# Optimization experiments

Measured on AMD Instinct MI355X. Metric: run time of the kernel, lower is better.

The kernel has to match this reference:

```python
import jax, jax.numpy as jnp
import numpy as np

N, E = 50000, 400000
F_IN, F_E = 128, 32
H, C = 4, 64          # heads, out_channels per head (concat=False -> head mean)
NUM_CLASSES = 16
BN_EPS = 1e-5


def setup_inputs() -> dict:
    key = jax.random.key(0)
    ks = jax.random.split(key, 16)
    s = 0.05
    return {
        "x": jax.random.normal(ks[0], (N, F_IN), jnp.float32),
        "edge_index": jax.random.randint(ks[1], (2, E), 0, N, jnp.int64),
        "edge_attr": jax.random.normal(ks[2], (E, F_E), jnp.float32),
        # TransformerConv params
        "Wq": jax.random.normal(ks[3], (F_IN, H * C), jnp.float32) * s,
        "bq": jnp.zeros((H * C,), jnp.float32),
        "Wk": jax.random.normal(ks[4], (F_IN, H * C), jnp.float32) * s,
        "bk": jnp.zeros((H * C,), jnp.float32),
        "Wv": jax.random.normal(ks[5], (F_IN, H * C), jnp.float32) * s,
        "bv": jnp.zeros((H * C,), jnp.float32),
        "We": jax.random.normal(ks[6], (F_E, H * C), jnp.float32) * s,  # lin_edge, no bias
        "Wskip": jax.random.normal(ks[7], (F_IN, C), jnp.float32) * s,   # root weight (concat=False -> C)
        "bskip": jnp.zeros((C,), jnp.float32),
        # BatchNorm1d (eval mode: running stats)
        "gamma": jnp.ones((C,), jnp.float32),
        "beta": jnp.zeros((C,), jnp.float32),
        "run_mean": jnp.zeros((C,), jnp.float32),
        "run_var": jnp.ones((C,), jnp.float32),
        # classifier
        "Wc": jax.random.normal(ks[8], (C, NUM_CLASSES), jnp.float32) * s,
        "bc": jnp.zeros((NUM_CLASSES,), jnp.float32),
    }


def reference(x, edge_index, edge_attr, Wq, bq, Wk, bk, Wv, bv, We,
              Wskip, bskip, gamma, beta, run_mean, run_var, Wc, bc):
    src = edge_index[0]  # j (message source)
    dst = edge_index[1]  # i (message target / softmax segment)

    q = (x @ Wq + bq).reshape(N, H, C)
    k = (x @ Wk + bk).reshape(N, H, C)
    v = (x @ Wv + bv).reshape(N, H, C)
    e = (edge_attr @ We).reshape(E, H, C)

    k_j = k[src] + e                                   # [E,H,C]
    score = jnp.sum(q[dst] * k_j, axis=-1) / jnp.sqrt(jnp.float32(C))  # [E,H]

    # segment softmax over incoming edges of each destination node
    m = jax.ops.segment_max(score, dst, num_segments=N)      # [N,H]
    ex = jnp.exp(score - m[dst])                             # [E,H]
    denom = jax.ops.segment_sum(ex, dst, num_segments=N)[dst]
    alpha = ex / denom                                       # [E,H]

    msg = (v[src] + e) * alpha[..., None]                    # [E,H,C]
    out = jax.ops.segment_sum(msg, dst, num_segments=N)      # [N,H,C]
    out = out.mean(axis=1)                                   # concat=False -> head mean [N,C]
    out = out + x @ Wskip + bskip                            # root/skip connection

    out = jax.nn.relu(out)
    # dropout: eval mode -> identity
    out = (out - run_mean) / jnp.sqrt(run_var + BN_EPS) * gamma + beta
    return out @ Wc + bc
```

## Files before the change

### kernel.cpp

```cpp
#include <hip/hip_runtime.h>
#include <hip/hip_bf16.h>

#define H 4
#define C 64
#define HC 256
#define FIN 128
#define FE 32
#define NCLS 16
#define BN_EPS 1e-5f
#define WCOLS 960

typedef __hip_bfloat16 bf16;
typedef __attribute__((ext_vector_type(8))) short short8v;
typedef __attribute__((ext_vector_type(4))) short short4v;
typedef __attribute__((ext_vector_type(2))) short short2v;
typedef __attribute__((ext_vector_type(4))) float floatx4;

__device__ __forceinline__ float b2f(bf16 v) { return __bfloat162float(v); }
__device__ __forceinline__ float bs2f(short s) {
    unsigned u = ((unsigned)(unsigned short)s) << 16;
    return __uint_as_float(u);
}
__device__ __forceinline__ short f2bs(float f) {
    bf16 h = __float2bfloat16(f);
    return *reinterpret_cast<short*>(&h);
}

__global__ __launch_bounds__(128) void pack_w_kernel(
    const float* __restrict__ Wq, const float* __restrict__ Wk, const float* __restrict__ Wv,
    const float* __restrict__ We, const float* __restrict__ Wskip,
    const float* __restrict__ bq, const float* __restrict__ bk, const float* __restrict__ bv,
    const float* __restrict__ bskip,
    const float* __restrict__ gamma, const float* __restrict__ beta,
    const float* __restrict__ rmean, const float* __restrict__ rvar,
    const float* __restrict__ Wc,
    short* __restrict__ Wt, float* __restrict__ bias,
    short* __restrict__ Wet, short* __restrict__ Wct,
    float* __restrict__ scalev, float* __restrict__ shiftv)
{
    const int bid = blockIdx.x;
    const int t = threadIdx.x;
    if (bid < WCOLS) {
        const int col = bid;
        float val, b = 0.f;
        if (col < 256)      { val = Wq[t * HC + col]; b = bq[col]; }
        else if (col < 512) { val = Wk[t * HC + col - 256]; b = bk[col - 256]; }
        else if (col < 768) { val = Wv[t * HC + col - 512]; b = bv[col - 512]; }
        else if (col < 896) {
            int j = col - 768, h = j >> 5, f = j & 31;
            float acc = 0.f;
#pragma unroll 8
            for (int c = 0; c < C; ++c) acc += Wq[t * HC + h * C + c] * We[f * HC + h * C + c];
            val = acc;
            acc = 0.f;
            for (int c = 0; c < C; ++c) acc += bq[h * C + c] * We[f * HC + h * C + c];
            b = acc;
        }
        else { int c2 = col - 896; val = Wskip[t * C + c2]; b = bskip[c2]; }
        Wt[(size_t)col * FIN + t] = f2bs(val);
        if (t == 0) bias[col] = b;
    } else if (bid < WCOLS + 64) {
        const int c2 = bid - WCOLS;
        const int f = t & 31, h = t >> 5;
        Wet[(size_t)c2 * FIN + t] = f2bs(We[f * HC + h * C + c2]);
    } else if (bid < WCOLS + 64 + NCLS) {
        const int cls = bid - WCOLS - 64;
        if (t < C) Wct[(size_t)cls * C + t] = f2bs(Wc[t * NCLS + cls]);
    } else {
        if (t < C) {
            float inv = rsqrtf(rvar[t] + BN_EPS);
            float sc = gamma[t] * inv;
            scalev[t] = sc;
            shiftv[t] = beta[t] - rmean[t] * sc;
        }
    }
}

__global__ __launch_bounds__(256) void qkv_mfma_kernel(
    const float* __restrict__ x, const short* __restrict__ Wt,
    const float* __restrict__ bias,
    bf16* __restrict__ q, unsigned char* __restrict__ kv,
    bf16* __restrict__ qWe, bf16* __restrict__ skip, int N)
{
    const int wid = threadIdx.x >> 6;
    const int lane = threadIdx.x & 63;
    const int n0 = blockIdx.x * 32;
    const int arow = lane & 15, agrp = lane >> 4;
    __shared__ __align__(16) unsigned char kvs[32][512];

    short8v afrag[2][4];
#pragma unroll
    for (int rt = 0; rt < 2; ++rt) {
        int nA = n0 + rt * 16 + arow; if (nA >= N) nA = N - 1;
        const float* xrow = x + (size_t)nA * FIN + agrp * 8;
#pragma unroll
        for (int ks = 0; ks < 4; ++ks) {
            floatx4 x0 = *(const floatx4*)(xrow + ks * 32);
            floatx4 x1 = *(const floatx4*)(xrow + ks * 32 + 4);
            short8v a;
            a[0] = f2bs(x0[0]); a[1] = f2bs(x0[1]); a[2] = f2bs(x0[2]); a[3] = f2bs(x0[3]);
            a[4] = f2bs(x1[0]); a[5] = f2bs(x1[1]); a[6] = f2bs(x1[2]); a[7] = f2bs(x1[3]);
            afrag[rt][ks] = a;
        }
    }

    for (int ct = wid; ct < WCOLS / 16; ct += 4) {
        const int col0 = ct * 16;
        const int col = col0 + arow;
        const short* wp = Wt + (size_t)col * FIN + agrp * 8;
        short8v bfr[4];
#pragma unroll
        for (int ks = 0; ks < 4; ++ks) bfr[ks] = *(const short8v*)(wp + ks * 32);
        floatx4 acc0 = {0.f, 0.f, 0.f, 0.f};
        floatx4 acc1 = {0.f, 0.f, 0.f, 0.f};
#pragma unroll
        for (int ks = 0; ks < 4; ++ks) {
            acc0 = __builtin_amdgcn_mfma_f32_16x16x32_bf16(afrag[0][ks], bfr[ks], acc0, 0, 0, 0);
            acc1 = __builtin_amdgcn_mfma_f32_16x16x32_bf16(afrag[1][ks], bfr[ks], acc1, 0, 0, 0);
        }
        const float bb = bias[col];
#pragma unroll
        for (int rt = 0; rt < 2; ++rt) {
            const floatx4 acc = rt ? acc1 : acc0;
#pragma unroll
            for (int r = 0; r < 4; ++r) {
                const int row = rt * 16 + agrp * 4 + r;
                const int n = n0 + row;
                const float val = acc[r] + bb;
                if (col0 >= 256 && col0 < 768) {
                    int c = col - 256;
                    const int isv = (c >= 256) ? 4 : 0;
                    c &= 255;
                    const int pos = ((c >> 6) * 16 + ((c & 63) >> 2)) * 8 + (c & 3) + isv;
                    const int p8 = __builtin_amdgcn_cvt_pk_fp8_f32(val, val, 0, false);
                    kvs[row][pos] = (unsigned char)(p8 & 0xff);
                } else if (n < N) {
                    if (col0 < 256)      q[(size_t)n * HC + col]          = __float2bfloat16(val);
                    else if (col0 < 896) qWe[(size_t)n * 128 + col - 768] = __float2bfloat16(val);
                    else                 skip[(size_t)n * C + col - 896]  = __float2bfloat16(val);
                }
            }
        }
    }
    __syncthreads();
    const int t = threadIdx.x;
#pragma unroll
    for (int it = 0; it < 4; ++it) {
        const int lin = it * 256 + t;
        const int row = lin >> 5;
        const int ch  = lin & 31;
        const int n = n0 + row;
        if (n < N)
            *(uint4*)(kv + (size_t)n * 512 + ch * 16) = *(const uint4*)(&kvs[row][ch * 16]);
    }
}

__global__ __launch_bounds__(256) void hist_kernel(
    const int* __restrict__ dst, int* __restrict__ deg, int E)
{
    const int i = blockIdx.x * 256 + threadIdx.x;
    if (i < E) atomicAdd(&deg[dst[i]], 1);
}

__global__ __launch_bounds__(256) void partial_kernel(
    const int* __restrict__ deg, int* __restrict__ partials, int N)
{
    const int t = threadIdx.x;
    const int base = blockIdx.x * 1024 + t * 4;
    int s = 0;
#pragma unroll
    for (int i = 0; i < 4; ++i) {
        int idx = base + i;
        if (idx < N) s += deg[idx];
    }
#pragma unroll
    for (int off = 1; off < 64; off <<= 1) s += __shfl_xor(s, off, 64);
    __shared__ int ws[4];
    if ((t & 63) == 0) ws[t >> 6] = s;
    __syncthreads();
    if (t == 0) partials[blockIdx.x] = ws[0] + ws[1] + ws[2] + ws[3];
}

__global__ __launch_bounds__(256) void scan_partials_kernel(
    int* __restrict__ partials, int* __restrict__ rowptr, int nb, int N)
{
    const int t = threadIdx.x;
    __shared__ int sm[256];
    int v = (t < nb) ? partials[t] : 0;
    sm[t] = v;
    __syncthreads();
    for (int off = 1; off < 256; off <<= 1) {
        int vv = (t >= off) ? sm[t - off] : 0;
        __syncthreads();
        sm[t] += vv;
        __syncthreads();
    }
    if (t < nb) partials[t] = sm[t] - v;
    if (t == 255) rowptr[N] = sm[255];
}

__global__ __launch_bounds__(256) void write_rowptr_kernel(
    const int* __restrict__ deg, const int* __restrict__ partials,
    int* __restrict__ rowptr, int N)
{
    const int t = threadIdx.x;
    const int base = blockIdx.x * 1024 + t * 4;
    int d[4];
    int s = 0;
#pragma unroll
    for (int i = 0; i < 4; ++i) {
        int idx = base + i;
        d[i] = (idx < N) ? deg[idx] : 0;
        s += d[i];
    }
    __shared__ int sm[256];
    sm[t] = s;
    __syncthreads();
    for (int off = 1; off < 256; off <<= 1) {
        int vv = (t >= off) ? sm[t - off] : 0;
        __syncthreads();
        sm[t] += vv;
        __syncthreads();
    }
    int run = partials[blockIdx.x] + sm[t] - s;
#pragma unroll
    for (int i = 0; i < 4; ++i) {
        int idx = base + i;
        if (idx < N) { rowptr[idx] = run; run += d[i]; }
    }
}

__global__ __launch_bounds__(256) void scatter_kernel(
    const int* __restrict__ src, const int* __restrict__ dst,
    const int* __restrict__ rowptr, int* __restrict__ cnt2,
    int2* __restrict__ edg, int E)
{
    const int i = blockIdx.x * 256 + threadIdx.x;
    if (i >= E) return;
    const int d = dst[i];
    const int pos = rowptr[d] + atomicAdd(&cnt2[d], 1);
    edg[pos] = make_int2(src[i], i);
}

__global__ __launch_bounds__(256) void node_agg_kernel(
    const int2* __restrict__ edg, const int* __restrict__ rowptr,
    const float* __restrict__ ea,
    const bf16* __restrict__ q, const unsigned char* __restrict__ kv,
    const bf16* __restrict__ qWe,
    bf16* __restrict__ accV, bf16* __restrict__ aggEA, int N)
{
    const int w = threadIdx.x >> 6;
    const int lane = threadIdx.x & 63;
    const int d = blockIdx.x * 4 + w;
    if (d >= N) return;
    const int g = lane >> 4;
    const int li = lane & 15;
    const int kvoff = (g * 16 + li) * 8;

    short4v qs = *(const short4v*)((const short*)q + (size_t)d * HC + g * C + li * 4);
    const float qv0 = bs2f(qs[0]), qv1 = bs2f(qs[1]), qv2 = bs2f(qs[2]), qv3 = bs2f(qs[3]);
    short2v qws = *(const short2v*)((const short*)qWe + (size_t)d * 128 + g * FE + li * 2);
    const float qw0 = bs2f(qws[0]), qw1 = bs2f(qws[1]);

    float den = 0.f;
    float a0 = 0.f, a1 = 0.f, a2 = 0.f, a3 = 0.f;
    float ag0 = 0.f, ag1 = 0.f;

    const int beg = rowptr[d];
    const int degc = rowptr[d + 1] - beg;

    for (int c0 = 0; c0 < degc; c0 += 64) {
        const int cnt = min(degc - c0, 64);
        int2 me = make_int2(0, 0);
        if (lane < cnt) me = edg[beg + c0 + lane];

        const int s0 = __builtin_amdgcn_readlane(me.x, 0);
        const int e0i = __builtin_amdgcn_readlane(me.y, 0);
        uint2 kvv = *(const uint2*)(kv + (size_t)s0 * 512 + kvoff);
        float2 eaf = *(const float2*)(ea + (size_t)e0i * FE + li * 2);

        for (int j = 0; j < cnt; ++j) {
            uint2 kvn = kvv; float2 ean = eaf;
            if (j + 1 < cnt) {
                const int sn = __builtin_amdgcn_readlane(me.x, j + 1);
                const int en = __builtin_amdgcn_readlane(me.y, j + 1);
                kvn = *(const uint2*)(kv + (size_t)sn * 512 + kvoff);
                ean = *(const float2*)(ea + (size_t)en * FE + li * 2);
            }
            const float ea0 = eaf.x, ea1 = eaf.y;
            const int klo = (int)kvv.x, vhi = (int)kvv.y;
            float p = qv0 * __builtin_amdgcn_cvt_f32_fp8(klo, 0)
                    + qv1 * __builtin_amdgcn_cvt_f32_fp8(klo, 1)
                    + qv2 * __builtin_amdgcn_cvt_f32_fp8(klo, 2)
                    + qv3 * __builtin_amdgcn_cvt_f32_fp8(klo, 3)
                    + qw0 * ea0 + qw1 * ea1;
            p += __shfl_xor(p, 1, 64);
            p += __shfl_xor(p, 2, 64);
            p += __shfl_xor(p, 4, 64);
            p += __shfl_xor(p, 8, 64);
            const float e = exp2f(p * 0.18033688f);
            den += e;
            a0 += e * __builtin_amdgcn_cvt_f32_fp8(vhi, 0);
            a1 += e * __builtin_amdgcn_cvt_f32_fp8(vhi, 1);
            a2 += e * __builtin_amdgcn_cvt_f32_fp8(vhi, 2);
            a3 += e * __builtin_amdgcn_cvt_f32_fp8(vhi, 3);
            ag0 += e * ea0; ag1 += e * ea1;
            kvv = kvn; eaf = ean;
        }
    }

    const float inv = den > 0.f ? 0.25f / den : 0.f;
    a0 *= inv; a1 *= inv; a2 *= inv; a3 *= inv;
    a0 += __shfl_xor(a0, 16, 64); a0 += __shfl_xor(a0, 32, 64);
    a1 += __shfl_xor(a1, 16, 64); a1 += __shfl_xor(a1, 32, 64);
    a2 += __shfl_xor(a2, 16, 64); a2 += __shfl_xor(a2, 32, 64);
    a3 += __shfl_xor(a3, 16, 64); a3 += __shfl_xor(a3, 32, 64);
    if (g == 0) {
        short4v o;
        o[0] = f2bs(a0); o[1] = f2bs(a1); o[2] = f2bs(a2); o[3] = f2bs(a3);
        *(short4v*)((short*)accV + (size_t)d * C + li * 4) = o;
    }
    short2v so;
    so[0] = f2bs(ag0 * inv);
    so[1] = f2bs(ag1 * inv);
    *(short2v*)((short*)aggEA + (size_t)d * 128 + g * FE + li * 2) = so;
}

__global__ __launch_bounds__(256) void final_kernel(
    const bf16* __restrict__ aggEA, const bf16* __restrict__ accV,
    const bf16* __restrict__ skip,
    const short* __restrict__ Wet, const short* __restrict__ Wct,
    const float* __restrict__ scalev, const float* __restrict__ shiftv,
    const float* __restrict__ bc,
    float* __restrict__ out, int N)
{
    const int wid = threadIdx.x >> 6;
    const int lane = threadIdx.x & 63;
    const int n0 = blockIdx.x * 16;
    const int arow = lane & 15, agrp = lane >> 4;
    __shared__ short hs[16][72];

    int nA = n0 + arow; if (nA >= N) nA = N - 1;
    const short* ap = (const short*)aggEA + (size_t)nA * 128 + agrp * 8;
    const int c0 = wid * 16;
    const int col = c0 + arow;
    const short* wp = Wet + (size_t)col * FIN + agrp * 8;
    floatx4 acc = {0.f, 0.f, 0.f, 0.f};
#pragma unroll
    for (int ks = 0; ks < 4; ++ks) {
        short8v a = *(const short8v*)(ap + ks * 32);
        short8v b = *(const short8v*)(wp + ks * 32);
        acc = __builtin_amdgcn_mfma_f32_16x16x32_bf16(a, b, acc, 0, 0, 0);
    }
    const float sc = scalev[col], sh = shiftv[col];
#pragma unroll
    for (int r = 0; r < 4; ++r) {
        const int row = agrp * 4 + r;
        int n = n0 + row; int nc = (n < N) ? n : (N - 1);
        float z = acc[r] + b2f(accV[(size_t)nc * C + col]) + b2f(skip[(size_t)nc * C + col]);
        z = fmaxf(z, 0.f);
        z = z * sc + sh;
        hs[row][col] = f2bs(z);
    }
    __syncthreads();

    if (wid == 0) {
        short8v ah[2], bh[2];
#pragma unroll
        for (int ks = 0; ks < 2; ++ks) {
#pragma unroll
            for (int j = 0; j < 8; ++j) ah[ks][j] = hs[arow][ks * 32 + agrp * 8 + j];
            bh[ks] = *(const short8v*)(Wct + (size_t)arow * C + ks * 32 + agrp * 8);
        }
        floatx4 co = {0.f, 0.f, 0.f, 0.f};
        co = __builtin_amdgcn_mfma_f32_16x16x32_bf16(ah[0], bh[0], co, 0, 0, 0);
        co = __builtin_amdgcn_mfma_f32_16x16x32_bf16(ah[1], bh[1], co, 0, 0, 0);
        const float bcv = bc[arow];
#pragma unroll
        for (int r = 0; r < 4; ++r) {
            const int n = n0 + agrp * 4 + r;
            if (n < N) out[(size_t)n * NCLS + arow] = co[r] + bcv;
        }
    }
}

extern "C" void kernel_launch(void* const* d_in, const int* in_sizes, int n_in,
                              void* d_out, int out_size, void* d_ws, size_t ws_size,
                              hipStream_t stream)
{
    const float* x     = (const float*)d_in[0];
    const int*   ei    = (const int*)d_in[1];
    const float* ea    = (const float*)d_in[2];
    const float* Wq    = (const float*)d_in[3];
    const float* bq    = (const float*)d_in[4];
    const float* Wk    = (const float*)d_in[5];
    const float* bk    = (const float*)d_in[6];
    const float* Wv    = (const float*)d_in[7];
    const float* bv    = (const float*)d_in[8];
    const float* We    = (const float*)d_in[9];
    const float* Wskip = (const float*)d_in[10];
    const float* bskip = (const float*)d_in[11];
    const float* gamma = (const float*)d_in[12];
    const float* beta  = (const float*)d_in[13];
    const float* rmean = (const float*)d_in[14];
    const float* rvar  = (const float*)d_in[15];
    const float* Wc    = (const float*)d_in[16];
    const float* bc    = (const float*)d_in[17];
    float* out = (float*)d_out;

    const int N = in_sizes[0] / FIN;
    const int E = in_sizes[2] / FE;
    const int* srcp = ei;
    const int* dstp = ei + E;
    const int nb = (N + 1023) / 1024;

    char* w = (char*)d_ws;
    size_t off = 0;
    auto alloc = [&](size_t bytes) { void* p = w + off; off += (bytes + 255) & ~255ull; return p; };
    bf16*  qb     = (bf16*)alloc((size_t)N * HC * sizeof(bf16));
    unsigned char* kvbuf = (unsigned char*)alloc((size_t)N * 512);
    bf16*  qWe    = (bf16*)alloc((size_t)N * 128 * sizeof(bf16));
    bf16*  skip   = (bf16*)alloc((size_t)N * C * sizeof(bf16));
    int*   deg    = (int*)alloc((size_t)N * sizeof(int));
    int*   rowptr = (int*)alloc((size_t)(N + 1) * sizeof(int));
    int*   cnt2   = (int*)alloc((size_t)N * sizeof(int));
    int*   partials = (int*)alloc(256 * sizeof(int));
    int2*  edg    = (int2*)alloc((size_t)E * sizeof(int2));
    bf16*  accV   = (bf16*)alloc((size_t)N * C * sizeof(bf16));
    bf16*  aggEA  = (bf16*)alloc((size_t)N * 128 * sizeof(bf16));
    short* Wt     = (short*)alloc((size_t)WCOLS * FIN * sizeof(short));
    float* bias   = (float*)alloc((size_t)WCOLS * sizeof(float));
    short* Wet    = (short*)alloc((size_t)C * FIN * sizeof(short));
    short* Wct    = (short*)alloc((size_t)NCLS * C * sizeof(short));
    float* scalev = (float*)alloc((size_t)C * sizeof(float));
    float* shiftv = (float*)alloc((size_t)C * sizeof(float));

    hipMemsetAsync(deg,  0, (size_t)N * sizeof(int), stream);
    hipMemsetAsync(cnt2, 0, (size_t)N * sizeof(int), stream);

    pack_w_kernel<<<WCOLS + 64 + NCLS + 1, 128, 0, stream>>>(
        Wq, Wk, Wv, We, Wskip, bq, bk, bv, bskip, gamma, beta, rmean, rvar, Wc,
        Wt, bias, Wet, Wct, scalev, shiftv);
    qkv_mfma_kernel<<<(N + 31) / 32, 256, 0, stream>>>(x, Wt, bias, qb, kvbuf, qWe, skip, N);
    hist_kernel<<<(E + 255) / 256, 256, 0, stream>>>(dstp, deg, E);
    partial_kernel<<<nb, 256, 0, stream>>>(deg, partials, N);
    scan_partials_kernel<<<1, 256, 0, stream>>>(partials, rowptr, nb, N);
    write_rowptr_kernel<<<nb, 256, 0, stream>>>(deg, partials, rowptr, N);
    scatter_kernel<<<(E + 255) / 256, 256, 0, stream>>>(srcp, dstp, rowptr, cnt2, edg, E);
    node_agg_kernel<<<(N + 3) / 4, 256, 0, stream>>>(edg, rowptr, ea, qb, kvbuf, qWe, accV, aggEA, N);
    final_kernel<<<(N + 15) / 16, 256, 0, stream>>>(aggEA, accV, skip, Wet, Wct, scalev, shiftv, bc, out, N);
}
```

Measured before the change: 198.7 us.

## Fuse degree histogram into QKV kernel and CSR build into cooperative kernel

Moves the destination-degree atomic histogram into the tail of the QKV MFMA kernel as a grid-stride loop. The partial sums, partials scan, rowptr write and edge scatter are merged into one cooperative kernel of 1024 blocks that uses grid-wide syncs. The goal is to remove five kernel launches and the idle gaps between them. In exchange, the grid syncs add cost and the cooperative launch requires all 1024 blocks to be resident at once.

```diff
diff --git a/kernel.cpp b/kernel.cpp
--- a/kernel.cpp
+++ b/kernel.cpp
@@ -1,5 +1,8 @@
 #include <hip/hip_runtime.h>
 #include <hip/hip_bf16.h>
+#include <hip/hip_cooperative_groups.h>
+
+namespace cg = cooperative_groups;
 
 #define H 4
 #define C 64
@@ -80,7 +83,8 @@
     const float* __restrict__ x, const short* __restrict__ Wt,
     const float* __restrict__ bias,
     bf16* __restrict__ q, unsigned char* __restrict__ kv,
-    bf16* __restrict__ qWe, bf16* __restrict__ skip, int N)
+    bf16* __restrict__ qWe, bf16* __restrict__ skip,
+    const int* __restrict__ dst, int* __restrict__ deg, int N, int E)
 {
     const int wid = threadIdx.x >> 6;
     const int lane = threadIdx.x & 63;
@@ -153,93 +157,88 @@
         if (n < N)
             *(uint4*)(kv + (size_t)n * 512 + ch * 16) = *(const uint4*)(&kvs[row][ch * 16]);
     }
-}
-
-__global__ __launch_bounds__(256) void hist_kernel(
-    const int* __restrict__ dst, int* __restrict__ deg, int E)
-{
-    const int i = blockIdx.x * 256 + threadIdx.x;
-    if (i < E) atomicAdd(&deg[dst[i]], 1);
-}
-
-__global__ __launch_bounds__(256) void partial_kernel(
-    const int* __restrict__ deg, int* __restrict__ partials, int N)
-{
+    const int gtid = blockIdx.x * 256 + t;
+    const int nth = gridDim.x * 256;
+    for (int i = gtid; i < E; i += nth) atomicAdd(&deg[dst[i]], 1);
+}
+
+__global__ __launch_bounds__(256) void csr_kernel(
+    const int* __restrict__ src, const int* __restrict__ dst,
+    const int* __restrict__ deg, int* __restrict__ partials,
+    int* __restrict__ rowptr, int* __restrict__ cnt2,
+    int2* __restrict__ edg, int N, int E)
+{
+    cg::grid_group grid = cg::this_grid();
     const int t = threadIdx.x;
-    const int base = blockIdx.x * 1024 + t * 4;
-    int s = 0;
-#pragma unroll
-    for (int i = 0; i < 4; ++i) {
-        int idx = base + i;
-        if (idx < N) s += deg[idx];
-    }
-#pragma unroll
-    for (int off = 1; off < 64; off <<= 1) s += __shfl_xor(s, off, 64);
+    const int nb = (N + 1023) >> 10;
     __shared__ int ws[4];
-    if ((t & 63) == 0) ws[t >> 6] = s;
-    __syncthreads();
-    if (t == 0) partials[blockIdx.x] = ws[0] + ws[1] + ws[2] + ws[3];
-}
-
-__global__ __launch_bounds__(256) void scan_partials_kernel(
-    int* __restrict__ partials, int* __restrict__ rowptr, int nb, int N)
-{
-    const int t = threadIdx.x;
     __shared__ int sm[256];
-    int v = (t < nb) ? partials[t] : 0;
-    sm[t] = v;
-    __syncthreads();
-    for (int off = 1; off < 256; off <<= 1) {
-        int vv = (t >= off) ? sm[t - off] : 0;
+
+    if ((int)blockIdx.x < nb) {
+        const int base = blockIdx.x * 1024 + t * 4;
+        int s = 0;
+#pragma unroll
+        for (int i = 0; i < 4; ++i) {
+            int idx = base + i;
+            if (idx < N) s += deg[idx];
+        }
+#pragma unroll
+        for (int off = 1; off < 64; off <<= 1) s += __shfl_xor(s, off, 64);
+        if ((t & 63) == 0) ws[t >> 6] = s;
         __syncthreads();
-        sm[t] += vv;
+        if (t == 0) partials[blockIdx.x] = ws[0] + ws[1] + ws[2] + ws[3];
+    }
+    grid.sync();
+
+    if (blockIdx.x == 0) {
+        int v = (t < nb) ? partials[t] : 0;
+        sm[t] = v;
         __syncthreads();
-    }
-    if (t < nb) partials[t] = sm[t] - v;
-    if (t == 255) rowptr[N] = sm[255];
-}
-
-__global__ __launch_bounds__(256) void write_rowptr_kernel(
-    const int* __restrict__ deg, const int* __restrict__ partials,
-    int* __restrict__ rowptr, int N)
-{
-    const int t = threadIdx.x;
-    const int base = blockIdx.x * 1024 + t * 4;
-    int d[4];
-    int s = 0;
-#pragma unroll
-    for (int i = 0; i < 4; ++i) {
-        int idx = base + i;
-        d[i] = (idx < N) ? deg[idx] : 0;
-        s += d[i];
-    }
-    __shared__ int sm[256];
-    sm[t] = s;
-    __syncthreads();
-    for (int off = 1; off < 256; off <<= 1) {
-        int vv = (t >= off) ? sm[t - off] : 0;
+        for (int off = 1; off < 256; off <<= 1) {
+            int vv = (t >= off) ? sm[t - off] : 0;
+            __syncthreads();
+            sm[t] += vv;
+            __syncthreads();
+        }
+        if (t < nb) partials[t] = sm[t] - v;
+        if (t == 255) rowptr[N] = sm[255];
+    }
+    grid.sync();
+
+    if ((int)blockIdx.x < nb) {
+        const int base = blockIdx.x * 1024 + t * 4;
+        int d[4];
+        int s = 0;
+#pragma unroll
+        for (int i = 0; i < 4; ++i) {
+            int idx = base + i;
+            d[i] = (idx < N) ? deg[idx] : 0;
+            s += d[i];
+        }
+        sm[t] = s;
         __syncthreads();
-        sm[t] += vv;
-        __syncthreads();
-    }
-    int run = partials[blockIdx.x] + sm[t] - s;
-#pragma unroll
-    for (int i = 0; i < 4; ++i) {
-        int idx = base + i;
-        if (idx < N) { rowptr[idx] = run; run += d[i]; }
-    }
-}
-
-__global__ __launch_bounds__(256) void scatter_kernel(
-    const int* __restrict__ src, const int* __restrict__ dst,
-    const int* __restrict__ rowptr, int* __restrict__ cnt2,
-    int2* __restrict__ edg, int E)
-{
-    const int i = blockIdx.x * 256 + threadIdx.x;
-    if (i >= E) return;
-    const int d = dst[i];
-    const int pos = rowptr[d] + atomicAdd(&cnt2[d], 1);
-    edg[pos] = make_int2(src[i], i);
+        for (int off = 1; off < 256; off <<= 1) {
+            int vv = (t >= off) ? sm[t - off] : 0;
+            __syncthreads();
+            sm[t] += vv;
+            __syncthreads();
+        }
+        int run = partials[blockIdx.x] + sm[t] - s;
+#pragma unroll
+        for (int i = 0; i < 4; ++i) {
+            int idx = base + i;
+            if (idx < N) { rowptr[idx] = run; run += d[i]; }
+        }
+    }
+    grid.sync();
+
+    const int gtid = blockIdx.x * 256 + t;
+    const int nth = gridDim.x * 256;
+    for (int i = gtid; i < E; i += nth) {
+        const int d = dst[i];
+        const int pos = rowptr[d] + atomicAdd(&cnt2[d], 1);
+        edg[pos] = make_int2(src[i], i);
+    }
 }
 
 __global__ __launch_bounds__(256) void node_agg_kernel(
@@ -412,7 +411,6 @@
     const int E = in_sizes[2] / FE;
     const int* srcp = ei;
     const int* dstp = ei + E;
-    const int nb = (N + 1023) / 1024;
 
     char* w = (char*)d_ws;
     size_t off = 0;
@@ -441,12 +439,16 @@
     pack_w_kernel<<<WCOLS + 64 + NCLS + 1, 128, 0, stream>>>(
         Wq, Wk, Wv, We, Wskip, bq, bk, bv, bskip, gamma, beta, rmean, rvar, Wc,
         Wt, bias, Wet, Wct, scalev, shiftv);
-    qkv_mfma_kernel<<<(N + 31) / 32, 256, 0, stream>>>(x, Wt, bias, qb, kvbuf, qWe, skip, N);
-    hist_kernel<<<(E + 255) / 256, 256, 0, stream>>>(dstp, deg, E);
-    partial_kernel<<<nb, 256, 0, stream>>>(deg, partials, N);
-    scan_partials_kernel<<<1, 256, 0, stream>>>(partials, rowptr, nb, N);
-    write_rowptr_kernel<<<nb, 256, 0, stream>>>(deg, partials, rowptr, N);
-    scatter_kernel<<<(E + 255) / 256, 256, 0, stream>>>(srcp, dstp, rowptr, cnt2, edg, E);
+    qkv_mfma_kernel<<<(N + 31) / 32, 256, 0, stream>>>(
+        x, Wt, bias, qb, kvbuf, qWe, skip, dstp, deg, N, E);
+
+    {
+        int Ni = N, Ei = E;
+        void* args[] = { (void*)&srcp, (void*)&dstp, (void*)&deg, (void*)&partials,
+                         (void*)&rowptr, (void*)&cnt2, (void*)&edg, (void*)&Ni, (void*)&Ei };
+        hipLaunchCooperativeKernel((void*)csr_kernel, dim3(1024), dim3(256), args, 0, stream);
+    }
+
     node_agg_kernel<<<(N + 3) / 4, 256, 0, stream>>>(edg, rowptr, ea, qb, kvbuf, qWe, accV, aggEA, N);
     final_kernel<<<(N + 15) / 16, 256, 0, stream>>>(aggEA, accV, skip, Wet, Wct, scalev, shiftv, bc, out, N);
 }
```

Measured after the change: 519.7 us. 162% more time.
